# Optimization experiments

Hardware: AMD Instinct MI355X
Metric: run time of the kernel (lower is better)

The kernel has to match this reference:

```python
import jax, jax.numpy as jnp
import numpy as np

N_NODES = 100000
E_HALF = 500000   # undirected pairs; mirrored to E = 1M directed edges
NFEAT = 128
NHID = 64
NCLASS = 40


def setup_inputs() -> dict:
    key = jax.random.key(0)
    ks = jax.random.split(key, 8)
    s = jax.random.randint(ks[0], (E_HALF,), 0, N_NODES, dtype=jnp.int32)
    off = jax.random.randint(ks[1], (E_HALF,), 1, N_NODES, dtype=jnp.int32)
    d = (s + off) % N_NODES  # no self-loops in the raw edge list
    src = jnp.concatenate([s, d])
    dst = jnp.concatenate([d, s])
    ar = jnp.arange(E_HALF, dtype=jnp.int32)
    rev = jnp.concatenate([ar + E_HALF, ar])  # index of reverse edge (j,i) for edge (i,j)
    x = jax.random.uniform(ks[2], (N_NODES, NFEAT), dtype=jnp.float32)
    W1 = jax.random.normal(ks[3], (NFEAT, NHID), jnp.float32) / np.sqrt(NFEAT).astype(np.float32)
    b1 = jnp.zeros((NHID,), jnp.float32)
    W2 = jax.random.normal(ks[4], (NHID, NCLASS), jnp.float32) / np.sqrt(NHID).astype(np.float32)
    b2 = jnp.zeros((NCLASS,), jnp.float32)
    Wd = jax.random.normal(ks[5], (2, 1), jnp.float32)
    bd = jax.random.normal(ks[6], (1,), jnp.float32) * 0.1
    return {"x": x, "src": src, "dst": dst, "rev": rev,
            "W1": W1, "b1": b1, "W2": W2, "b2": b2, "Wd": Wd, "bd": bd}


def att_coef(f, src, dst, rev, n, Wd, bd, mask):
    """Edge-list version of GuardGCN.att_coef (drop=True).
    mask zeroes edges removed by a previous att_coef pass.
    Returns (per-edge weights [E], per-node self-loop weights [n])."""
    nrm = jnp.sqrt(jnp.sum(f * f, axis=1))
    safe = jnp.where(nrm == 0, 1.0, nrm)
    # cosine similarity only on the listed edges (diagonal handled via lam below)
    sim = jnp.sum(f[src] * f[dst], axis=1) / (safe[src] * safe[dst])
    sim = jnp.where(sim < 0.1, 0.0, sim) * mask
    # L1 row normalization (sklearn normalize(axis=1, norm='l1'))
    rowsum = jax.ops.segment_sum(jnp.abs(sim), src, num_segments=n)
    a = sim / jnp.where(rowsum == 0, 1.0, rowsum)[src]
    # learnable drop: Linear(2,1) on [a_ij, a_ji] -> sigmoid -> binary keep at 0.5
    char = jnp.stack([a, a[rev]], axis=1)  # [E, 2]
    keep = jax.nn.sigmoid(char @ Wd + bd)[:, 0] > 0.5
    a = jnp.where(keep, a, 0.0)
    # self-loop weight lam_i = 1 / (deg_i + 1), deg = surviving out-edges
    deg = jax.ops.segment_sum((a != 0).astype(f.dtype), src, num_segments=n)
    lam = 1.0 / (deg + 1.0)
    # exp() applied only to nonzero entries (zeros are absent in sparse nonzero())
    w_e = jnp.where(a > 0, jnp.exp(a), 0.0)
    w_s = jnp.exp(lam)
    return w_e, w_s


def gcn_conv(h, src, dst, w, n, W, b):
    """torch_geometric GCNConv: gcn_norm (add self-loops fill=1, sym D^-1/2 A D^-1/2),
    then aggregate h @ W along edges (src -> dst) and add bias."""
    h = h @ W
    iota = jnp.arange(n, dtype=src.dtype)
    src2 = jnp.concatenate([src, iota])
    dst2 = jnp.concatenate([dst, iota])
    w2 = jnp.concatenate([w, jnp.ones((n,), h.dtype)])
    deg = jax.ops.segment_sum(w2, dst2, num_segments=n)
    dis = jnp.where(deg > 0, deg ** -0.5, 0.0)
    norm = dis[src2] * w2 * dis[dst2]
    out = jax.ops.segment_sum(norm[:, None] * h[src2], dst2, num_segments=n)
    return out + b


def reference(x, src, dst, rev, W1, b1, W2, b2, Wd, bd):
    n = x.shape[0]
    iota = jnp.arange(n, dtype=src.dtype)
    # layer-0 attention on raw features
    w_e1, w_s1 = att_coef(x, src, dst, rev, n, Wd, bd, jnp.ones(src.shape, x.dtype))
    src_f = jnp.concatenate([src, iota])
    dst_f = jnp.concatenate([dst, iota])
    w_f1 = jnp.concatenate([w_e1, w_s1])
    h = jax.nn.relu(gcn_conv(x, src_f, dst_f, w_f1, n, W1, b1))
    # layer-1 attention on hidden features; edge set = survivors of pass 0
    mask1 = (w_e1 > 0).astype(x.dtype)
    w_e2, w_s2 = att_coef(h, src, dst, rev, n, Wd, bd, mask1)
    w_f2 = jnp.concatenate([w_e2, w_s2])
    # dropout is identity in eval mode
    out = gcn_conv(h, src_f, dst_f, w_f2, n, W2, b2)
    return jax.nn.log_softmax(out, axis=1)
```

## Files before the change

### kernel.cpp

```cpp
#include <hip/hip_runtime.h>

#define N_NODES 100000
#define E_HALF  500000
#define E_TOT   1000000
#define NFEAT   128
#define NHID    64
#define NCLS    40
#define SCAN_T  1024
#define SCAN_NB 98

__device__ __forceinline__ int REV(int e) { return (e < E_HALF) ? e + E_HALF : e - E_HALF; }

template<int D>
__global__ __launch_bounds__(256) void row_norm_k(const float* __restrict__ x, float* __restrict__ nrm) {
    int w = (blockIdx.x * 256 + threadIdx.x) >> 6;
    int lane = threadIdx.x & 63;
    if (w >= N_NODES) return;
    const float* row = x + (size_t)w * D;
    float s = 0.f;
#pragma unroll
    for (int i = 0; i < D / 64; ++i) { float v = row[lane + 64 * i]; s = fmaf(v, v, s); }
#pragma unroll
    for (int off = 32; off; off >>= 1) s += __shfl_xor(s, off);
    if (lane == 0) nrm[w] = sqrtf(s);
}

template<int D, bool MASKED>
__global__ __launch_bounds__(256) void sim_k(const float* __restrict__ f, const float* __restrict__ nrm,
                                             const int* __restrict__ src, const int* __restrict__ dst,
                                             const float* __restrict__ we_mask,
                                             float* __restrict__ sim) {
    int g = blockIdx.x * 256 + threadIdx.x;
    int ep = g >> 4, sl = g & 15;
    if (ep >= E_HALF) return;
    bool m0 = true, m1 = true;
    if (MASKED) {
        m0 = we_mask[ep] > 0.f;
        m1 = we_mask[ep + E_HALF] > 0.f;
        if (!m0 && !m1) {
            if (sl == 0) { sim[ep] = 0.f; sim[ep + E_HALF] = 0.f; }
            return;
        }
    }
    int s = src[ep], d = dst[ep];
    const float* fa = f + (size_t)s * D + sl * (D / 16);
    const float* fb = f + (size_t)d * D + sl * (D / 16);
    float acc = 0.f;
#pragma unroll
    for (int i = 0; i < D / 16; i += 4) {
        float4 va = *(const float4*)(fa + i);
        float4 vb = *(const float4*)(fb + i);
        acc = fmaf(va.x, vb.x, acc); acc = fmaf(va.y, vb.y, acc);
        acc = fmaf(va.z, vb.z, acc); acc = fmaf(va.w, vb.w, acc);
    }
    acc += __shfl_xor(acc, 8); acc += __shfl_xor(acc, 4);
    acc += __shfl_xor(acc, 2); acc += __shfl_xor(acc, 1);
    if (sl == 0) {
        float na = nrm[s]; na = (na == 0.f) ? 1.f : na;
        float nb = nrm[d]; nb = (nb == 0.f) ? 1.f : nb;
        float c = acc / (na * nb);
        float t = (c < 0.1f) ? 0.f : c;
        sim[ep]          = m0 ? t : 0.f;
        sim[ep + E_HALF] = m1 ? t : 0.f;
    }
}

__global__ __launch_bounds__(256) void rowsum_k(const float* __restrict__ sim, const int* __restrict__ row_start,
                                                const int* __restrict__ csr_eid, float* __restrict__ rowsum) {
    int g = blockIdx.x * 256 + threadIdx.x;
    int j = g >> 2, l = g & 3;
    if (j >= N_NODES) return;
    int e0 = row_start[j], e1 = row_start[j + 1];
    float s = 0.f;
    for (int t = e0 + l; t < e1; t += 4) s += sim[csr_eid[t]];
    s += __shfl_xor(s, 1); s += __shfl_xor(s, 2);
    if (l == 0) rowsum[j] = s;
}

__global__ __launch_bounds__(256) void keep_k(const float* __restrict__ sim,
                                              const int* __restrict__ src, const int* __restrict__ dst,
                                              const float* __restrict__ rowsum,
                                              const float* __restrict__ Wd, const float* __restrict__ bd,
                                              float* __restrict__ we) {
    int e = blockIdx.x * 256 + threadIdx.x;
    if (e >= E_TOT) return;
    int s = src[e], d = dst[e];
    float rs = rowsum[s]; rs = (rs == 0.f) ? 1.f : rs;
    float rd = rowsum[d]; rd = (rd == 0.f) ? 1.f : rd;
    float ae = sim[e] / rs;
    float ar = sim[REV(e)] / rd;
    float z = ae * Wd[0] + ar * Wd[1] + bd[0];
    float av = (z > 0.f) ? ae : 0.f;
    we[e] = (av > 0.f) ? expf(av) : 0.f;
}

__global__ __launch_bounds__(256) void nodeB_k(const float* __restrict__ we, const int* __restrict__ row_start,
                                               const int* __restrict__ csr_eid,
                                               float* __restrict__ w_s, float* __restrict__ dis) {
    int g = blockIdx.x * 256 + threadIdx.x;
    int j = g >> 2, l = g & 3;
    if (j >= N_NODES) return;
    int e0 = row_start[j], e1 = row_start[j + 1];
    float c = 0.f, s = 0.f;
    for (int t = e0 + l; t < e1; t += 4) {
        int eid = csr_eid[t];
        c += (we[eid] > 0.f) ? 1.f : 0.f;
        s += we[REV(eid)];
    }
    c += __shfl_xor(c, 1); c += __shfl_xor(c, 2);
    s += __shfl_xor(s, 1); s += __shfl_xor(s, 2);
    if (l == 0) {
        float ws = expf(1.f / (c + 1.f));
        w_s[j] = ws;
        dis[j] = 1.f / sqrtf(s + ws + 1.f);
    }
}

__global__ __launch_bounds__(256) void count_k(const int* __restrict__ src, int* __restrict__ cnt) {
    int e = blockIdx.x * 256 + threadIdx.x;
    if (e < E_TOT) atomicAdd(&cnt[src[e]], 1);
}

__global__ __launch_bounds__(1024) void scan1_k(const int* __restrict__ cnt, int* __restrict__ bsum) {
    int i = blockIdx.x * SCAN_T + threadIdx.x;
    int v = (i < N_NODES) ? cnt[i] : 0;
#pragma unroll
    for (int off = 32; off; off >>= 1) v += __shfl_xor(v, off);
    __shared__ int wsm[16];
    int lane = threadIdx.x & 63, wid = threadIdx.x >> 6;
    if (lane == 0) wsm[wid] = v;
    __syncthreads();
    if (threadIdx.x == 0) {
        int s = 0;
#pragma unroll
        for (int k = 0; k < 16; ++k) s += wsm[k];
        bsum[blockIdx.x] = s;
    }
}

__global__ __launch_bounds__(128) void scan2_k(int* __restrict__ bsum) {
    __shared__ int tmp[128];
    int t = threadIdx.x;
    int v = (t < SCAN_NB) ? bsum[t] : 0;
    tmp[t] = v;
    __syncthreads();
    for (int off = 1; off < 128; off <<= 1) {
        int add = (t >= off) ? tmp[t - off] : 0;
        __syncthreads();
        tmp[t] += add;
        __syncthreads();
    }
    if (t < SCAN_NB) bsum[t] = (t > 0) ? tmp[t - 1] : 0;
}

__global__ __launch_bounds__(1024) void scan3_k(const int* __restrict__ cnt, const int* __restrict__ bsum,
                                                int* __restrict__ row_start) {
    int i = blockIdx.x * SCAN_T + threadIdx.x;
    int v = (i < N_NODES) ? cnt[i] : 0;
    int lane = threadIdx.x & 63, wid = threadIdx.x >> 6;
    int x = v;
#pragma unroll
    for (int off = 1; off < 64; off <<= 1) {
        int y = __shfl_up(x, off);
        if (lane >= off) x += y;
    }
    __shared__ int wsum[16], woff[16];
    if (lane == 63) wsum[wid] = x;
    __syncthreads();
    if (threadIdx.x == 0) {
        int s = 0;
#pragma unroll
        for (int k = 0; k < 16; ++k) { woff[k] = s; s += wsum[k]; }
    }
    __syncthreads();
    int excl = (x - v) + woff[wid] + bsum[blockIdx.x];
    if (i < N_NODES) row_start[i] = excl;
    if (i == N_NODES - 1) row_start[N_NODES] = excl + v;
}

__global__ __launch_bounds__(256) void fill_k(const int* __restrict__ src, const int* __restrict__ dst,
                                              const int* __restrict__ row_start, int* __restrict__ cursor,
                                              int* __restrict__ csr_col, int* __restrict__ csr_eid) {
    int e = blockIdx.x * 256 + threadIdx.x;
    if (e >= E_TOT) return;
    int s = src[e];
    int p = atomicAdd(&cursor[s], 1);
    int slot = row_start[s] + p;
    csr_col[slot] = dst[e];
    csr_eid[slot] = e;
}

__global__ __launch_bounds__(256) void slotw_k(const int* __restrict__ csr_col, const int* __restrict__ csr_eid,
                                               const float* __restrict__ we, const float* __restrict__ dis,
                                               float* __restrict__ wsl) {
    int t = blockIdx.x * 256 + threadIdx.x;
    if (t >= E_TOT) return;
    wsl[t] = dis[csr_col[t]] * we[REV(csr_eid[t])];
}

__global__ __launch_bounds__(256) void gemm1_k(const float* __restrict__ X, const float* __restrict__ W,
                                               float* __restrict__ Y) {
    __shared__ float sXT[8][128];
    __shared__ float sW[8][64];
    int tid = threadIdx.x;
    int row0 = blockIdx.x * 128;
    int tc = tid & 15;
    int tr = tid >> 4;
    float acc[8][4] = {};
    int lrow = tid >> 1, lhalf = tid & 1;
    int grow = row0 + lrow;
    for (int k0 = 0; k0 < NFEAT; k0 += 8) {
        float4 v = make_float4(0.f, 0.f, 0.f, 0.f);
        if (grow < N_NODES) v = *(const float4*)(X + (size_t)grow * NFEAT + k0 + lhalf * 4);
        sXT[lhalf * 4 + 0][lrow] = v.x;
        sXT[lhalf * 4 + 1][lrow] = v.y;
        sXT[lhalf * 4 + 2][lrow] = v.z;
        sXT[lhalf * 4 + 3][lrow] = v.w;
        float2 wv2 = *(const float2*)(W + (size_t)(k0 + (tid >> 5)) * NHID + (tid & 31) * 2);
        *(float2*)&sW[tid >> 5][(tid & 31) * 2] = wv2;
        __syncthreads();
#pragma unroll
        for (int k = 0; k < 8; ++k) {
            float4 xa = *(const float4*)&sXT[k][tr * 8];
            float4 xb = *(const float4*)&sXT[k][tr * 8 + 4];
            float4 wv = *(const float4*)&sW[k][tc * 4];
            float xr[8] = {xa.x, xa.y, xa.z, xa.w, xb.x, xb.y, xb.z, xb.w};
            float wr[4] = {wv.x, wv.y, wv.z, wv.w};
#pragma unroll
            for (int i = 0; i < 8; ++i)
#pragma unroll
                for (int jj = 0; jj < 4; ++jj)
                    acc[i][jj] = fmaf(xr[i], wr[jj], acc[i][jj]);
        }
        __syncthreads();
    }
#pragma unroll
    for (int i = 0; i < 8; ++i) {
        int r = row0 + tr * 8 + i;
        if (r < N_NODES)
            *(float4*)(Y + (size_t)r * NHID + tc * 4) =
                make_float4(acc[i][0], acc[i][1], acc[i][2], acc[i][3]);
    }
}

__global__ __launch_bounds__(256) void gemm2_k(const float* __restrict__ X, const float* __restrict__ W,
                                               float* __restrict__ Y) {
    __shared__ float sXT[8][128];
    __shared__ float sW[320];
    int tid = threadIdx.x;
    int row0 = blockIdx.x * 128;
    int tc = tid & 7;
    int tr = tid >> 3;
    float acc[4][5] = {};
    int lrow = tid >> 1, lhalf = tid & 1;
    int grow = row0 + lrow;
    for (int k0 = 0; k0 < NHID; k0 += 8) {
        float4 v = make_float4(0.f, 0.f, 0.f, 0.f);
        if (grow < N_NODES) v = *(const float4*)(X + (size_t)grow * NHID + k0 + lhalf * 4);
        sXT[lhalf * 4 + 0][lrow] = v.x;
        sXT[lhalf * 4 + 1][lrow] = v.y;
        sXT[lhalf * 4 + 2][lrow] = v.z;
        sXT[lhalf * 4 + 3][lrow] = v.w;
        if (tid < 160) {
            float2 w2 = *(const float2*)(W + k0 * NCLS + tid * 2);
            sW[tid * 2] = w2.x; sW[tid * 2 + 1] = w2.y;
        }
        __syncthreads();
#pragma unroll
        for (int k = 0; k < 8; ++k) {
            float4 xv = *(const float4*)&sXT[k][tr * 4];
            float xr[4] = {xv.x, xv.y, xv.z, xv.w};
            float wr[5];
#pragma unroll
            for (int jj = 0; jj < 5; ++jj) wr[jj] = sW[k * NCLS + tc * 5 + jj];
#pragma unroll
            for (int i = 0; i < 4; ++i)
#pragma unroll
                for (int jj = 0; jj < 5; ++jj)
                    acc[i][jj] = fmaf(xr[i], wr[jj], acc[i][jj]);
        }
        __syncthreads();
    }
#pragma unroll
    for (int i = 0; i < 4; ++i) {
        int r = row0 + tr * 4 + i;
        if (r < N_NODES) {
#pragma unroll
            for (int jj = 0; jj < 5; ++jj) Y[(size_t)r * NCLS + tc * 5 + jj] = acc[i][jj];
        }
    }
}

__global__ __launch_bounds__(256) void agg1_k(const float* __restrict__ hpre, const int* __restrict__ row_start,
                                              const int* __restrict__ csr_col, const float* __restrict__ wsl,
                                              const float* __restrict__ dis, const float* __restrict__ w_s,
                                              const float* __restrict__ b, float* __restrict__ h) {
    int j = (blockIdx.x * 256 + threadIdx.x) >> 6;
    int lane = threadIdx.x & 63;
    if (j >= N_NODES) return;
    int e0 = row_start[j], e1 = row_start[j + 1];
    float acc = 0.f;
    int t = e0;
    for (; t + 4 <= e1; t += 4) {
        int s0 = csr_col[t], s1 = csr_col[t + 1], s2 = csr_col[t + 2], s3 = csr_col[t + 3];
        float w0 = wsl[t], w1 = wsl[t + 1], w2 = wsl[t + 2], w3 = wsl[t + 3];
        float v0 = hpre[(size_t)s0 * NHID + lane];
        float v1 = hpre[(size_t)s1 * NHID + lane];
        float v2 = hpre[(size_t)s2 * NHID + lane];
        float v3 = hpre[(size_t)s3 * NHID + lane];
        acc = fmaf(w0, v0, acc); acc = fmaf(w1, v1, acc);
        acc = fmaf(w2, v2, acc); acc = fmaf(w3, v3, acc);
    }
    for (; t < e1; ++t)
        acc = fmaf(wsl[t], hpre[(size_t)csr_col[t] * NHID + lane], acc);
    float dj = dis[j];
    acc = fmaf(dj * (w_s[j] + 1.f), hpre[(size_t)j * NHID + lane], acc);
    float v = fmaf(acc, dj, b[lane]);
    h[(size_t)j * NHID + lane] = fmaxf(v, 0.f);
}

__global__ __launch_bounds__(256) void agg2_k(const float* __restrict__ hp2, const int* __restrict__ row_start,
                                              const int* __restrict__ csr_col, const float* __restrict__ wsl,
                                              const float* __restrict__ dis, const float* __restrict__ w_s,
                                              const float* __restrict__ b, float* __restrict__ out) {
    int j = (blockIdx.x * 256 + threadIdx.x) >> 6;
    int lane = threadIdx.x & 63;
    if (j >= N_NODES) return;
    int lc = (lane < NCLS) ? lane : (NCLS - 1);
    int e0 = row_start[j], e1 = row_start[j + 1];
    float acc = 0.f;
    int t = e0;
    for (; t + 4 <= e1; t += 4) {
        int s0 = csr_col[t], s1 = csr_col[t + 1], s2 = csr_col[t + 2], s3 = csr_col[t + 3];
        float w0 = wsl[t], w1 = wsl[t + 1], w2 = wsl[t + 2], w3 = wsl[t + 3];
        float v0 = hp2[(size_t)s0 * NCLS + lc];
        float v1 = hp2[(size_t)s1 * NCLS + lc];
        float v2 = hp2[(size_t)s2 * NCLS + lc];
        float v3 = hp2[(size_t)s3 * NCLS + lc];
        acc = fmaf(w0, v0, acc); acc = fmaf(w1, v1, acc);
        acc = fmaf(w2, v2, acc); acc = fmaf(w3, v3, acc);
    }
    for (; t < e1; ++t)
        acc = fmaf(wsl[t], hp2[(size_t)csr_col[t] * NCLS + lc], acc);
    float dj = dis[j];
    acc = fmaf(dj * (w_s[j] + 1.f), hp2[(size_t)j * NCLS + lc], acc);
    float v = (lane < NCLS) ? fmaf(acc, dj, b[lane]) : -1e30f;
    float m = v;
#pragma unroll
    for (int off = 32; off; off >>= 1) m = fmaxf(m, __shfl_xor(m, off));
    float ex = (lane < NCLS) ? expf(v - m) : 0.f;
    float ssum = ex;
#pragma unroll
    for (int off = 32; off; off >>= 1) ssum += __shfl_xor(ssum, off);
    if (lane < NCLS) out[(size_t)j * NCLS + lane] = v - m - logf(ssum);
}

extern "C" void kernel_launch(void* const* d_in, const int* in_sizes, int n_in,
                              void* d_out, int out_size, void* d_ws, size_t ws_size,
                              hipStream_t stream) {
    (void)in_sizes; (void)n_in; (void)out_size; (void)ws_size;
    const float* x  = (const float*)d_in[0];
    const int*   src = (const int*)d_in[1];
    const int*   dst = (const int*)d_in[2];
    const float* W1 = (const float*)d_in[4];
    const float* b1 = (const float*)d_in[5];
    const float* W2 = (const float*)d_in[6];
    const float* b2 = (const float*)d_in[7];
    const float* Wd = (const float*)d_in[8];
    const float* bd = (const float*)d_in[9];
    float* out = (float*)d_out;

    char* ws = (char*)d_ws;
    size_t off = 0;
    auto alloc = [&](size_t bytes) -> void* {
        void* p = ws + off;
        off = (off + bytes + 255) & ~(size_t)255;
        return p;
    };
    int*   cnt    = (int*)alloc((size_t)N_NODES * 4);
    float* nrm    = (float*)alloc((size_t)N_NODES * 4);
    float* rowsum = (float*)alloc((size_t)N_NODES * 4);
    float* w_s    = (float*)alloc((size_t)N_NODES * 4);
    float* dis    = (float*)alloc((size_t)N_NODES * 4);
    float* sbuf   = (float*)alloc((size_t)E_TOT * 4);
    float* we1    = (float*)alloc((size_t)E_TOT * 4);
    float* we2    = (float*)alloc((size_t)E_TOT * 4);
    float* wsl    = (float*)alloc((size_t)E_TOT * 4);
    float* hpre   = (float*)alloc((size_t)N_NODES * NHID * 4);
    float* h      = (float*)alloc((size_t)N_NODES * NHID * 4);
    int* row_start = (int*)alloc((size_t)(N_NODES + 1) * 4);
    int* csr_col   = (int*)alloc((size_t)E_TOT * 4);
    int* csr_eid   = (int*)alloc((size_t)E_TOT * 4);
    int* bsum      = (int*)alloc(256 * 4);

    const int BE = (E_TOT + 255) / 256;
    const int BW = (N_NODES * 64 + 255) / 256;
    const int BQ = (N_NODES * 4 + 255) / 256;
    const int BS = (E_HALF * 16 + 255) / 256;
    const int BG = (N_NODES + 127) / 128;

    hipMemsetAsync(cnt, 0, (size_t)N_NODES * 4, stream);
    count_k<<<BE, 256, 0, stream>>>(src, cnt);
    scan1_k<<<SCAN_NB, 1024, 0, stream>>>(cnt, bsum);
    scan2_k<<<1, 128, 0, stream>>>(bsum);
    scan3_k<<<SCAN_NB, 1024, 0, stream>>>(cnt, bsum, row_start);
    hipMemsetAsync(cnt, 0, (size_t)N_NODES * 4, stream);
    fill_k<<<BE, 256, 0, stream>>>(src, dst, row_start, cnt, csr_col, csr_eid);

    row_norm_k<NFEAT><<<BW, 256, 0, stream>>>(x, nrm);
    sim_k<NFEAT, false><<<BS, 256, 0, stream>>>(x, nrm, src, dst, nullptr, sbuf);
    rowsum_k<<<BQ, 256, 0, stream>>>(sbuf, row_start, csr_eid, rowsum);
    keep_k<<<BE, 256, 0, stream>>>(sbuf, src, dst, rowsum, Wd, bd, we1);
    nodeB_k<<<BQ, 256, 0, stream>>>(we1, row_start, csr_eid, w_s, dis);
    gemm1_k<<<BG, 256, 0, stream>>>(x, W1, hpre);
    slotw_k<<<BE, 256, 0, stream>>>(csr_col, csr_eid, we1, dis, wsl);
    agg1_k<<<BW, 256, 0, stream>>>(hpre, row_start, csr_col, wsl, dis, w_s, b1, h);

    row_norm_k<NHID><<<BW, 256, 0, stream>>>(h, nrm);
    sim_k<NHID, true><<<BS, 256, 0, stream>>>(h, nrm, src, dst, we1, sbuf);
    rowsum_k<<<BQ, 256, 0, stream>>>(sbuf, row_start, csr_eid, rowsum);
    keep_k<<<BE, 256, 0, stream>>>(sbuf, src, dst, rowsum, Wd, bd, we2);
    nodeB_k<<<BQ, 256, 0, stream>>>(we2, row_start, csr_eid, w_s, dis);
    gemm2_k<<<BG, 256, 0, stream>>>(h, W2, hpre);
    slotw_k<<<BE, 256, 0, stream>>>(csr_col, csr_eid, we2, dis, wsl);
    agg2_k<<<BW, 256, 0, stream>>>(hpre, row_start, csr_col, wsl, dis, w_s, b2, out);
}
```

Measured before the change: 609.3 us.

## Interleave CSR col/eid, fuse slot weights into aggregation and row norm into agg1

Stores the CSR column and edge id together as one int2 array, so each slot fetches both indices in a single load. The slot-weight kernel is removed: the aggregation kernels now compute dis[col]*we[rev(eid)] inline, which drops two launches and a 1M-entry intermediate write and read. The layer-2 row-norm kernel is folded into agg1 as a wavefront reduction over the freshly written hidden row. In exchange, the aggregation loops issue extra scattered gathers of dis and we per edge, and the other CSR kernels now read 8-byte entries where they used only the eid.

New measurement: 591.9 us. -2.8%, faster.

```diff
diff --git a/kernel.cpp b/kernel.cpp
--- a/kernel.cpp
+++ b/kernel.cpp
@@ -66,13 +66,13 @@
 }
 
 __global__ __launch_bounds__(256) void rowsum_k(const float* __restrict__ sim, const int* __restrict__ row_start,
-                                                const int* __restrict__ csr_eid, float* __restrict__ rowsum) {
+                                                const int2* __restrict__ csr, float* __restrict__ rowsum) {
     int g = blockIdx.x * 256 + threadIdx.x;
     int j = g >> 2, l = g & 3;
     if (j >= N_NODES) return;
     int e0 = row_start[j], e1 = row_start[j + 1];
     float s = 0.f;
-    for (int t = e0 + l; t < e1; t += 4) s += sim[csr_eid[t]];
+    for (int t = e0 + l; t < e1; t += 4) s += sim[csr[t].y];
     s += __shfl_xor(s, 1); s += __shfl_xor(s, 2);
     if (l == 0) rowsum[j] = s;
 }
@@ -95,7 +95,7 @@
 }
 
 __global__ __launch_bounds__(256) void nodeB_k(const float* __restrict__ we, const int* __restrict__ row_start,
-                                               const int* __restrict__ csr_eid,
+                                               const int2* __restrict__ csr,
                                                float* __restrict__ w_s, float* __restrict__ dis) {
     int g = blockIdx.x * 256 + threadIdx.x;
     int j = g >> 2, l = g & 3;
@@ -103,7 +103,7 @@
     int e0 = row_start[j], e1 = row_start[j + 1];
     float c = 0.f, s = 0.f;
     for (int t = e0 + l; t < e1; t += 4) {
-        int eid = csr_eid[t];
+        int eid = csr[t].y;
         c += (we[eid] > 0.f) ? 1.f : 0.f;
         s += we[REV(eid)];
     }
@@ -180,22 +180,12 @@
 
 __global__ __launch_bounds__(256) void fill_k(const int* __restrict__ src, const int* __restrict__ dst,
                                               const int* __restrict__ row_start, int* __restrict__ cursor,
-                                              int* __restrict__ csr_col, int* __restrict__ csr_eid) {
+                                              int2* __restrict__ csr) {
     int e = blockIdx.x * 256 + threadIdx.x;
     if (e >= E_TOT) return;
     int s = src[e];
     int p = atomicAdd(&cursor[s], 1);
-    int slot = row_start[s] + p;
-    csr_col[slot] = dst[e];
-    csr_eid[slot] = e;
-}
-
-__global__ __launch_bounds__(256) void slotw_k(const int* __restrict__ csr_col, const int* __restrict__ csr_eid,
-                                               const float* __restrict__ we, const float* __restrict__ dis,
-                                               float* __restrict__ wsl) {
-    int t = blockIdx.x * 256 + threadIdx.x;
-    if (t >= E_TOT) return;
-    wsl[t] = dis[csr_col[t]] * we[REV(csr_eid[t])];
+    csr[row_start[s] + p] = make_int2(dst[e], e);
 }
 
 __global__ __launch_bounds__(256) void gemm1_k(const float* __restrict__ X, const float* __restrict__ W,
@@ -292,9 +282,10 @@
 }
 
 __global__ __launch_bounds__(256) void agg1_k(const float* __restrict__ hpre, const int* __restrict__ row_start,
-                                              const int* __restrict__ csr_col, const float* __restrict__ wsl,
+                                              const int2* __restrict__ csr, const float* __restrict__ we,
                                               const float* __restrict__ dis, const float* __restrict__ w_s,
-                                              const float* __restrict__ b, float* __restrict__ h) {
+                                              const float* __restrict__ b, float* __restrict__ h,
+                                              float* __restrict__ nrm) {
     int j = (blockIdx.x * 256 + threadIdx.x) >> 6;
     int lane = threadIdx.x & 63;
     if (j >= N_NODES) return;
@@ -302,25 +293,34 @@
     float acc = 0.f;
     int t = e0;
     for (; t + 4 <= e1; t += 4) {
-        int s0 = csr_col[t], s1 = csr_col[t + 1], s2 = csr_col[t + 2], s3 = csr_col[t + 3];
-        float w0 = wsl[t], w1 = wsl[t + 1], w2 = wsl[t + 2], w3 = wsl[t + 3];
-        float v0 = hpre[(size_t)s0 * NHID + lane];
-        float v1 = hpre[(size_t)s1 * NHID + lane];
-        float v2 = hpre[(size_t)s2 * NHID + lane];
-        float v3 = hpre[(size_t)s3 * NHID + lane];
+        int2 c0 = csr[t], c1 = csr[t + 1], c2 = csr[t + 2], c3 = csr[t + 3];
+        float w0 = dis[c0.x] * we[REV(c0.y)];
+        float w1 = dis[c1.x] * we[REV(c1.y)];
+        float w2 = dis[c2.x] * we[REV(c2.y)];
+        float w3 = dis[c3.x] * we[REV(c3.y)];
+        float v0 = hpre[(size_t)c0.x * NHID + lane];
+        float v1 = hpre[(size_t)c1.x * NHID + lane];
+        float v2 = hpre[(size_t)c2.x * NHID + lane];
+        float v3 = hpre[(size_t)c3.x * NHID + lane];
         acc = fmaf(w0, v0, acc); acc = fmaf(w1, v1, acc);
         acc = fmaf(w2, v2, acc); acc = fmaf(w3, v3, acc);
     }
-    for (; t < e1; ++t)
-        acc = fmaf(wsl[t], hpre[(size_t)csr_col[t] * NHID + lane], acc);
+    for (; t < e1; ++t) {
+        int2 c = csr[t];
+        acc = fmaf(dis[c.x] * we[REV(c.y)], hpre[(size_t)c.x * NHID + lane], acc);
+    }
     float dj = dis[j];
     acc = fmaf(dj * (w_s[j] + 1.f), hpre[(size_t)j * NHID + lane], acc);
-    float v = fmaf(acc, dj, b[lane]);
-    h[(size_t)j * NHID + lane] = fmaxf(v, 0.f);
+    float v = fmaxf(fmaf(acc, dj, b[lane]), 0.f);
+    h[(size_t)j * NHID + lane] = v;
+    float s = v * v;
+#pragma unroll
+    for (int off = 32; off; off >>= 1) s += __shfl_xor(s, off);
+    if (lane == 0) nrm[j] = sqrtf(s);
 }
 
 __global__ __launch_bounds__(256) void agg2_k(const float* __restrict__ hp2, const int* __restrict__ row_start,
-                                              const int* __restrict__ csr_col, const float* __restrict__ wsl,
+                                              const int2* __restrict__ csr, const float* __restrict__ we,
                                               const float* __restrict__ dis, const float* __restrict__ w_s,
                                               const float* __restrict__ b, float* __restrict__ out) {
     int j = (blockIdx.x * 256 + threadIdx.x) >> 6;
@@ -331,17 +331,22 @@
     float acc = 0.f;
     int t = e0;
     for (; t + 4 <= e1; t += 4) {
-        int s0 = csr_col[t], s1 = csr_col[t + 1], s2 = csr_col[t + 2], s3 = csr_col[t + 3];
-        float w0 = wsl[t], w1 = wsl[t + 1], w2 = wsl[t + 2], w3 = wsl[t + 3];
-        float v0 = hp2[(size_t)s0 * NCLS + lc];
-        float v1 = hp2[(size_t)s1 * NCLS + lc];
-        float v2 = hp2[(size_t)s2 * NCLS + lc];
-        float v3 = hp2[(size_t)s3 * NCLS + lc];
+        int2 c0 = csr[t], c1 = csr[t + 1], c2 = csr[t + 2], c3 = csr[t + 3];
+        float w0 = dis[c0.x] * we[REV(c0.y)];
+        float w1 = dis[c1.x] * we[REV(c1.y)];
+        float w2 = dis[c2.x] * we[REV(c2.y)];
+        float w3 = dis[c3.x] * we[REV(c3.y)];
+        float v0 = hp2[(size_t)c0.x * NCLS + lc];
+        float v1 = hp2[(size_t)c1.x * NCLS + lc];
+        float v2 = hp2[(size_t)c2.x * NCLS + lc];
+        float v3 = hp2[(size_t)c3.x * NCLS + lc];
         acc = fmaf(w0, v0, acc); acc = fmaf(w1, v1, acc);
         acc = fmaf(w2, v2, acc); acc = fmaf(w3, v3, acc);
     }
-    for (; t < e1; ++t)
-        acc = fmaf(wsl[t], hp2[(size_t)csr_col[t] * NCLS + lc], acc);
+    for (; t < e1; ++t) {
+        int2 c = csr[t];
+        acc = fmaf(dis[c.x] * we[REV(c.y)], hp2[(size_t)c.x * NCLS + lc], acc);
+    }
     float dj = dis[j];
     acc = fmaf(dj * (w_s[j] + 1.f), hp2[(size_t)j * NCLS + lc], acc);
     float v = (lane < NCLS) ? fmaf(acc, dj, b[lane]) : -1e30f;
@@ -385,13 +390,11 @@
     float* sbuf   = (float*)alloc((size_t)E_TOT * 4);
     float* we1    = (float*)alloc((size_t)E_TOT * 4);
     float* we2    = (float*)alloc((size_t)E_TOT * 4);
-    float* wsl    = (float*)alloc((size_t)E_TOT * 4);
     float* hpre   = (float*)alloc((size_t)N_NODES * NHID * 4);
     float* h      = (float*)alloc((size_t)N_NODES * NHID * 4);
-    int* row_start = (int*)alloc((size_t)(N_NODES + 1) * 4);
-    int* csr_col   = (int*)alloc((size_t)E_TOT * 4);
-    int* csr_eid   = (int*)alloc((size_t)E_TOT * 4);
-    int* bsum      = (int*)alloc(256 * 4);
+    int*  row_start = (int*)alloc((size_t)(N_NODES + 1) * 4);
+    int2* csr       = (int2*)alloc((size_t)E_TOT * 8);
+    int*  bsum      = (int*)alloc(256 * 4);
 
     const int BE = (E_TOT + 255) / 256;
     const int BW = (N_NODES * 64 + 255) / 256;
@@ -405,23 +408,20 @@
     scan2_k<<<1, 128, 0, stream>>>(bsum);
     scan3_k<<<SCAN_NB, 1024, 0, stream>>>(cnt, bsum, row_start);
     hipMemsetAsync(cnt, 0, (size_t)N_NODES * 4, stream);
-    fill_k<<<BE, 256, 0, stream>>>(src, dst, row_start, cnt, csr_col, csr_eid);
+    fill_k<<<BE, 256, 0, stream>>>(src, dst, row_start, cnt, csr);
 
     row_norm_k<NFEAT><<<BW, 256, 0, stream>>>(x, nrm);
     sim_k<NFEAT, false><<<BS, 256, 0, stream>>>(x, nrm, src, dst, nullptr, sbuf);
-    rowsum_k<<<BQ, 256, 0, stream>>>(sbuf, row_start, csr_eid, rowsum);
+    rowsum_k<<<BQ, 256, 0, stream>>>(sbuf, row_start, csr, rowsum);
     keep_k<<<BE, 256, 0, stream>>>(sbuf, src, dst, rowsum, Wd, bd, we1);
-    nodeB_k<<<BQ, 256, 0, stream>>>(we1, row_start, csr_eid, w_s, dis);
+    nodeB_k<<<BQ, 256, 0, stream>>>(we1, row_start, csr, w_s, dis);
     gemm1_k<<<BG, 256, 0, stream>>>(x, W1, hpre);
-    slotw_k<<<BE, 256, 0, stream>>>(csr_col, csr_eid, we1, dis, wsl);
-    agg1_k<<<BW, 256, 0, stream>>>(hpre, row_start, csr_col, wsl, dis, w_s, b1, h);
-
-    row_norm_k<NHID><<<BW, 256, 0, stream>>>(h, nrm);
+    agg1_k<<<BW, 256, 0, stream>>>(hpre, row_start, csr, we1, dis, w_s, b1, h, nrm);
+
     sim_k<NHID, true><<<BS, 256, 0, stream>>>(h, nrm, src, dst, we1, sbuf);
-    rowsum_k<<<BQ, 256, 0, stream>>>(sbuf, row_start, csr_eid, rowsum);
+    rowsum_k<<<BQ, 256, 0, stream>>>(sbuf, row_start, csr, rowsum);
     keep_k<<<BE, 256, 0, stream>>>(sbuf, src, dst, rowsum, Wd, bd, we2);
-    nodeB_k<<<BQ, 256, 0, stream>>>(we2, row_start, csr_eid, w_s, dis);
+    nodeB_k<<<BQ, 256, 0, stream>>>(we2, row_start, csr, w_s, dis);
     gemm2_k<<<BG, 256, 0, stream>>>(h, W2, hpre);
-    slotw_k<<<BE, 256, 0, stream>>>(csr_col, csr_eid, we2, dis, wsl);
-    agg2_k<<<BW, 256, 0, stream>>>(hpre, row_start, csr_col, wsl, dis, w_s, b2, out);
-}
+    agg2_k<<<BW, 256, 0, stream>>>(hpre, row_start, csr, we2, dis, w_s, b2, out);
+}
```
